# Kernel optimization log

Measured on AMD Instinct MI355X. Metric: run time of the kernel, lower is better.

Reference implementation:

```python
import jax, jax.numpy as jnp
import numpy as np

NEG_INF = float('-inf')


def setup_inputs() -> dict:
    key = jax.random.key(0)
    k1, k2, k3 = jax.random.split(key, 3)
    B, V = 256, 128000
    logits = jax.random.normal(k1, (B, V), dtype=jnp.float32) * 4.0
    # per-row top-k in [1, V]; k == V means top-k disabled for that row
    k = jax.random.randint(k2, (B,), 1, V + 1, dtype=jnp.int32)
    # per-row top-p in a realistic sampling range
    p = jax.random.uniform(k3, (B,), dtype=jnp.float32, minval=0.5, maxval=0.99)
    return {"logits": logits, "k": k, "p": p}


def reference(logits, k, p):
    """Faithful JAX port of vLLM apply_top_k_top_p (sort-based fallback).

    logits: [B, V] float32; k: [B] int (1..V, V => no top-k); p: [B] float (0,1].
    Returns masked logits [B, V] with filtered entries set to -inf.
    """
    B, V = logits.shape
    # ascending sort, as in torch: logits.sort(dim=-1, descending=False)
    idx = jnp.argsort(logits, axis=-1)                       # [B, V]
    logits_sort = jnp.take_along_axis(logits, idx, axis=-1)  # [B, V]

    # ---- top-k: threshold is the (V-k)-th smallest value; k==V -> idx 0 -> min,
    # so nothing is masked (strict '<' comparison), matching torch semantics.
    tk_idx = (V - k).astype(jnp.int32)[:, None]              # [B, 1]
    tk_thresh = jnp.take_along_axis(logits_sort, tk_idx, axis=-1)
    logits_sort = jnp.where(logits_sort < tk_thresh, NEG_INF, logits_sort)

    # ---- top-p: drop smallest-probability prefix with cumulative mass <= 1-p
    probs = jax.nn.softmax(logits_sort, axis=-1)
    top_p_mask = jnp.cumsum(probs, axis=-1) <= (1.0 - p)[:, None]
    top_p_mask = top_p_mask.at[:, -1].set(False)  # always keep the max logit
    logits_sort = jnp.where(top_p_mask, NEG_INF, logits_sort)

    # scatter masked sorted logits back to original positions (idx is a permutation)
    out = jnp.zeros_like(logits).at[jnp.arange(B)[:, None], idx].set(logits_sort)
    return out
```

## Files before the change

kernel.cpp:

```cpp
#include <hip/hip_runtime.h>

typedef unsigned long long u64;
typedef unsigned u32;
typedef float f32x4 __attribute__((ext_vector_type(4)));

#define VDIM   128000
#define NF4    32000
#define NROWS  256
#define NB     2048
#define NSEG   16
#define SEGW   768
#define CAPTOT (NSEG*SEGW)
#define CAPCHK 12288
#define CNTSH  47
#define EMASK  ((1ull<<CNTSH)-1ull)

#define MASKED_VAL -1.0e38f

__device__ __forceinline__ u32 f2key(float x){
  u32 u=__float_as_uint(x);
  return (u&0x80000000u)? ~u : (u|0x80000000u);
}
__device__ __forceinline__ float key2f(u32 k){
  u32 u=(k&0x80000000u)?(k&0x7FFFFFFFu):~k;
  return __uint_as_float(u);
}
__device__ __forceinline__ u64 expfx(float x){
  return (u64)(__expf(x)*8192.0f);
}

template<typename T>
__device__ __forceinline__ void block_scan_lds(T* a,int n){
  __shared__ T wsum[16];
  const int tid=threadIdx.x, lane=tid&63, wid=tid>>6;
  __syncthreads();
  const int chunk=n>>4;
  const int base=wid*chunk;
  T carry=(T)0;
  for(int c=0;c<chunk;c+=64){
    T v=a[base+c+lane];
    #pragma unroll
    for(int s=1;s<64;s<<=1){T t=__shfl_up(v,(unsigned)s);if(lane>=s)v+=t;}
    v+=carry;
    a[base+c+lane]=v;
    carry=__shfl(v,63);
  }
  if(lane==0)wsum[wid]=carry;
  __syncthreads();
  if(tid<64){
    T v=(tid<16)?wsum[tid]:(T)0;
    #pragma unroll
    for(int s=1;s<16;s<<=1){T t=__shfl_up(v,(unsigned)s);if(lane>=s)v+=t;}
    if(tid<16)wsum[tid]=v;
  }
  __syncthreads();
  if(wid>0){
    T off=wsum[wid-1];
    for(int c=0;c<chunk;c+=64)a[base+c+lane]+=off;
  }
  __syncthreads();
}

__device__ void gather(const float4* src,u32* ent,u32* wc,u32* fl,
                       int binA,int lo,int hi){
  const int tid=threadIdx.x, wid=tid>>6;
  if(tid<NSEG)wc[tid]=0u;
  if(tid==0){fl[0]=0u;fl[1]=0u;}
  __syncthreads();
  u32* seg=ent+wid*SEGW;
  for(int base=tid;base<NF4;base+=8192){
    float4 buf[8];
    #pragma unroll
    for(int u=0;u<8;u++){int i=base+u*1024;if(i<NF4)buf[u]=src[i];}
    #pragma unroll
    for(int u=0;u<8;u++){
      int i=base+u*1024;
      if(i<NF4){
        float xs[4]={buf[u].x,buf[u].y,buf[u].z,buf[u].w};
        #pragma unroll
        for(int c=0;c<4;c++){
          u32 key=f2key(xs[c]);
          int bin=(int)(key>>21);
          if(bin==binA||(bin>=lo&&bin<=hi)){
            u32 pos=atomicAdd(&wc[wid],1u);
            if(pos<SEGW)seg[pos]=key;
          }
        }
      }
    }
  }
  __syncthreads();
  if(tid<NSEG&&wc[tid]>(u32)SEGW)atomicOr(&fl[0],1u);
  __syncthreads();
  if(fl[0]){
    if(tid<NSEG)wc[tid]=0u;
    __syncthreads();
    for(int base=tid;base<NF4;base+=8192){
      float4 buf[8];
      #pragma unroll
      for(int u=0;u<8;u++){int i=base+u*1024;if(i<NF4)buf[u]=src[i];}
      #pragma unroll
      for(int u=0;u<8;u++){
        int i=base+u*1024;
        if(i<NF4){
          float xs[4]={buf[u].x,buf[u].y,buf[u].z,buf[u].w};
          #pragma unroll
          for(int c=0;c<4;c++){
            u32 key=f2key(xs[c]);
            int bin=(int)(key>>21);
            if(bin==binA||(bin>=lo&&bin<=hi)){
              u32 off=atomicAdd(&fl[1],1u);
              if(off<(u32)CAPTOT)ent[off]=key;
            }
          }
        }
      }
    }
    __syncthreads();
    if(tid<NSEG){
      int n=(int)min(fl[1],(u32)CAPTOT);
      int c0=n-tid*SEGW; c0=c0<0?0:(c0>SEGW?SEGW:c0);
      wc[tid]=(u32)c0;
    }
    __syncthreads();
  }else{
    __syncthreads();
  }
}

__device__ void refine_p(const float4* src,const u32* ent,const u32* wc,
                         u64* hR,int* si,u64* sw,
                         int bp,int bk,u32 K,u64 P0,double target,
                         u32* KPo,int* jso){
  const int tid=threadIdx.x;
  const bool fK=(bp==bk);
  if(tid==0){si[0]=-1;si[1]=-1;si[2]=0;si[5]=0;}
  for(int i=tid;i<NB;i+=1024)hR[i]=0ull;
  __syncthreads();
  for(int s=0;s<NSEG;s++){
    const int cN=(int)wc[s]; const u32* sp=ent+s*SEGW;
    for(int t=tid;t<cN;t+=1024){
      u32 key=sp[t];
      if((int)(key>>21)==bp&&(!fK||key>=K))
        atomicAdd(&hR[(key>>10)&0x7FFu],expfx(key2f(key)));
    }
  }
  block_scan_lds(hR,NB);
  for(int b=tid;b<NB;b+=1024){
    u64 cpre=P0+(b?hR[b-1]:0ull), cumb=P0+hR[b];
    if((double)cpre<=target&&target<(double)cumb){si[0]=b;sw[0]=cpre;}
  }
  __syncthreads();
  bool maskall=false;
  int b2=si[0];
  if(b2<0){
    maskall=true;
    for(int b=tid;b<NB;b+=1024){u64 pm=b?hR[b-1]:0ull;if(hR[b]>pm)atomicMax(&si[0],b);}
    __syncthreads();
    b2=si[0];
    if(tid==0&&b2>=0)sw[0]=P0+(b2>0?hR[b2-1]:0ull);
    __syncthreads();
    if(b2<0){*KPo=0u;*jso=-1;return;}
  }
  const u64 S2=sw[0];
  __syncthreads();
  hR[tid]=0ull;
  __syncthreads();
  for(int s=0;s<NSEG;s++){
    const int cN=(int)wc[s]; const u32* sp=ent+s*SEGW;
    for(int t=tid;t<cN;t+=1024){
      u32 key=sp[t];
      if((int)(key>>21)==bp&&(!fK||key>=K)&&(int)((key>>10)&0x7FFu)==b2)
        atomicAdd(&hR[key&0x3FFu],expfx(key2f(key)));
    }
  }
  block_scan_lds(hR,1024);
  if(!maskall&&tid<1024){
    u64 cpre=S2+(tid?hR[tid-1]:0ull), cumb=S2+hR[tid];
    if((double)cpre<=target&&target<(double)cumb)si[1]=tid;
  }
  __syncthreads();
  int low=si[1];
  if(low<0){
    maskall=true;
    if(tid<1024){u64 pm=tid?hR[tid-1]:0ull;if(hR[tid]>pm)atomicMax(&si[1],tid);}
    __syncthreads();
    low=si[1];
    if(low<0){*KPo=0u;*jso=-1;return;}
  }
  const u64 S3=S2+(low?hR[low-1]:0ull);
  const u32 KP=((u32)bp<<21)|((u32)b2<<10)|(u32)low;
  for(int s=0;s<NSEG;s++){
    const int cN=(int)wc[s]; const u32* sp=ent+s*SEGW;
    for(int t=tid;t<cN;t+=1024)if(sp[t]==KP)atomicAdd(&si[2],1);
  }
  __syncthreads();
  const int mm=min(si[2],4096);
  const u64 efx=expfx(key2f(KP));
  int r;
  if(maskall)r=mm;
  else if(efx==0ull)r=0;
  else{
    double f=(target-(double)S3)/(double)efx;
    r=(f<0.0)?0:(int)f;
    if(r>mm)r=mm;
  }
  int js=-1;
  if(r>0){
    __syncthreads();
    u32* tb=(u32*)hR;
    for(int i=tid;i<NF4;i+=1024){
      float4 v=src[i];
      float xs[4]={v.x,v.y,v.z,v.w};
      #pragma unroll
      for(int c=0;c<4;c++){
        if(f2key(xs[c])==KP){int pos=atomicAdd(&si[5],1);if(pos<2048)tb[pos]=(u32)(4*i+c);}
      }
    }
    __syncthreads();
    const int mc=min(si[5],2048);
    if(tid==0){
      if(r>=mc){
        u32 mx=0u;for(int q=0;q<mc;q++)mx=max(mx,tb[q]);
        si[3]=(int)mx;
      }else{
        int last=-1;
        for(int t2=0;t2<r;t2++){
          u32 mn=0xFFFFFFFFu;
          for(int q=0;q<mc;q++){u32 vi=tb[q];if((int)vi>last&&vi<mn)mn=vi;}
          last=(int)mn;
        }
        si[3]=last;
      }
    }
    __syncthreads();
    js=si[3];
  }
  if(tid==0)si[4]=(int)KP;
  __syncthreads();
  *KPo=(u32)si[4];*jso=js;
}

__global__ __launch_bounds__(1024) void k_fused(const float* __restrict__ lg,
    const int* __restrict__ karr,const float* __restrict__ parr,
    float* __restrict__ out){
  __shared__ u64 hA[NB];
  __shared__ u64 hR[NB];
  __shared__ u32 ent[CAPTOT];
  __shared__ u32 wc[NSEG];
  __shared__ u32 fl[2];
  __shared__ int si[12];
  __shared__ u64 sw[4];
  const int row=blockIdx.x, tid=threadIdx.x;
  const float4* src=(const float4*)(lg+(size_t)row*VDIM);

  for(int i=tid;i<NB;i+=1024)hA[i]=0ull;
  if(tid==0){si[0]=-1;si[1]=NB;si[2]=NB;si[3]=-1;si[4]=-1;si[5]=-1;}
  __syncthreads();
  for(int base=tid;base<NF4;base+=8192){
    float4 buf[8];
    #pragma unroll
    for(int u=0;u<8;u++){int i=base+u*1024;if(i<NF4)buf[u]=src[i];}
    #pragma unroll
    for(int u=0;u<8;u++){
      int i=base+u*1024;
      if(i<NF4){
        float xs[4]={buf[u].x,buf[u].y,buf[u].z,buf[u].w};
        #pragma unroll
        for(int c=0;c<4;c++){
          u32 key=f2key(xs[c]);
          atomicAdd(&hA[key>>21],(1ull<<CNTSH)+expfx(xs[c]));
        }
      }
    }
  }
  block_scan_lds(hA,NB);
  const int vk=VDIM-karr[row];
  for(int b=tid;b<NB;b+=1024){
    int pm1=b?(int)(hA[b-1]>>CNTSH):0, cm=(int)(hA[b]>>CNTSH);
    if(pm1<=vk&&vk<cm)si[0]=b;
  }
  __syncthreads();
  const int bk=si[0];
  const u64 Ebk=hA[bk]&EMASK;
  const u64 Ebkm1=bk?(hA[bk-1]&EMASK):0ull;
  const u64 Etot=hA[NB-1]&EMASK;
  const u64 tail=Etot-Ebk, Mbk=Ebk-Ebkm1;
  const int cntbk=(int)(hA[bk]>>CNTSH)-(bk?(int)(hA[bk-1]>>CNTSH):0);
  const int kprime=(int)(hA[bk]>>CNTSH)-vk;
  const float p=parr[row];
  const double th_max=(double)(1.0f-p)*(double)tail+(double)Ebk;
  const double th_min=th_max-(double)p*(double)Mbk;
  for(int b=tid;b<NB;b+=1024){
    double Eb=(double)(hA[b]&EMASK);
    if(Eb>th_min)atomicMin(&si[1],b);
    if(Eb>th_max)atomicMin(&si[2],b);
  }
  __syncthreads();
  int lo=si[1],hi=si[2];
  if(lo>=NB)lo=NB-1;
  if(hi>=NB)hi=NB-1;
  lo=max(bk,lo-1); hi=min(NB-1,hi+1); if(hi<lo)hi=lo;
  long long cr=(long long)(hA[hi]>>CNTSH)-(lo?(long long)(hA[lo-1]>>CNTSH):0ll);
  long long tot=cr+((lo==bk)?0ll:(long long)cntbk);
  const int comb=(tot<=(long long)CAPCHK)?1:0;
  gather(src,ent,wc,fl,bk,comb?lo:1,comb?hi:0);
  for(int i=tid;i<NB;i+=1024)hR[i]=0ull;
  __syncthreads();
  for(int s=0;s<NSEG;s++){
    const int cN=(int)wc[s]; const u32* sp=ent+s*SEGW;
    for(int t=tid;t<cN;t+=1024){
      u32 key=sp[t];
      if((int)(key>>21)==bk)
        atomicAdd(&hR[(key>>10)&0x7FFu],(1ull<<CNTSH)+expfx(key2f(key)));
    }
  }
  block_scan_lds(hR,NB);
  int t2=cntbk-kprime;if(t2<0)t2=0;
  for(int b=tid;b<NB;b+=1024){
    int pm1=b?(int)(hR[b-1]>>CNTSH):0, cm=(int)(hR[b]>>CNTSH);
    if(pm1<=t2&&t2<cm)si[3]=b;
  }
  __syncthreads();
  const int b2=(si[3]<0)?0:si[3];
  const int k2v=(int)(hR[b2]>>CNTSH)-t2;
  const u64 E2above=(hR[NB-1]&EMASK)-(hR[b2]&EMASK);
  __syncthreads();
  hR[tid]=0ull;
  __syncthreads();
  for(int s=0;s<NSEG;s++){
    const int cN=(int)wc[s]; const u32* sp=ent+s*SEGW;
    for(int t=tid;t<cN;t+=1024){
      u32 key=sp[t];
      if((int)(key>>21)==bk&&(int)((key>>10)&0x7FFu)==b2)
        atomicAdd(&hR[key&0x3FFu],(1ull<<CNTSH)+expfx(key2f(key)));
    }
  }
  block_scan_lds(hR,1024);
  const int nb2=(int)(hR[1023]>>CNTSH);
  int t3=nb2-k2v;if(t3<0)t3=0;
  if(tid<1024){
    int pm1=tid?(int)(hR[tid-1]>>CNTSH):0, cm=(int)(hR[tid]>>CNTSH);
    if(pm1<=t3&&t3<cm)si[4]=tid;
  }
  __syncthreads();
  const int lowk=(si[4]<0)?0:si[4];
  const u32 K=((u32)bk<<21)|((u32)b2<<10)|(u32)lowk;
  const u64 E3above=(hR[1023]&EMASK)-(lowk?(hR[lowk-1]&EMASK):0ull);
  const u64 kept=E2above+E3above;
  const double target=(double)(1.0f-p)*(double)(kept+tail);
  __syncthreads();
  for(int b=bk+tid;b<NB;b+=1024){
    u64 cpre=(b==bk)?0ull:(kept+((hA[b-1]&EMASK)-Ebk));
    u64 cumb=kept+((b>bk)?((hA[b]&EMASK)-Ebk):0ull);
    if((double)cpre<=target&&target<(double)cumb){si[5]=b;sw[0]=cpre;}
  }
  __syncthreads();
  const int bp=si[5];
  u32 KP=0u; int js=-1;
  if(bp>=0){
    const u64 P0=sw[0];
    const bool inset=(bp==bk)||(comb&&bp>=lo&&bp<=hi);
    if(!inset){
      __syncthreads();
      gather(src,ent,wc,fl,bp,1,0);
    }
    refine_p(src,ent,wc,hR,si+6,sw+1,bp,bk,K,P0,target,&KP,&js);
  }
  __syncthreads();
  f32x4* dst=(f32x4*)(out+(size_t)row*VDIM);
  for(int base=tid;base<NF4;base+=8192){
    float4 buf[8];
    #pragma unroll
    for(int u=0;u<8;u++){int i=base+u*1024;if(i<NF4)buf[u]=src[i];}
    #pragma unroll
    for(int u=0;u<8;u++){
      int i=base+u*1024;
      if(i<NF4){
        float xs[4]={buf[u].x,buf[u].y,buf[u].z,buf[u].w};
        f32x4 o;
        #pragma unroll
        for(int c=0;c<4;c++){
          u32 key=f2key(xs[c]);
          bool msk=(key<K)||(key<KP)||(key==KP&&(int)(4*i+c)<=js);
          o[c]=msk?MASKED_VAL:xs[c];
        }
        __builtin_nontemporal_store(o,dst+i);
      }
    }
  }
}

extern "C" void kernel_launch(void* const* d_in,const int* in_sizes,int n_in,
                              void* d_out,int out_size,void* d_ws,size_t ws_size,
                              hipStream_t stream){
  const float* lg=(const float*)d_in[0];
  const int*   karr=(const int*)d_in[1];
  const float* parr=(const float*)d_in[2];
  float* out=(float*)d_out;
  (void)d_ws;(void)ws_size;(void)in_sizes;(void)n_in;(void)out_size;
  k_fused<<<dim3(NROWS),dim3(1024),0,stream>>>(lg,karr,parr,out);
}
```

Measured before the change: 119.5 us.

## Fuse speculative output write into gather pass and fix up candidates only

In the combined case, the candidate-gather pass now also writes the output row. Elements in bins below the candidate range are written as masked, and all others are written unchanged. Candidate positions are kept in a new shared-memory array. When the final top-p threshold bin lies inside the gathered range, the closing full read-and-write pass is replaced by a scatter that rewrites only the candidate entries. This removes one full read of each row from global memory in the common case. It costs an extra 48KB of LDS and scattered, uncoalesced writes that overwrite values just stored by other threads.

```diff
diff --git a/kernel.cpp b/kernel.cpp
--- a/kernel.cpp
+++ b/kernel.cpp
@@ -61,13 +61,14 @@
   __syncthreads();
 }
 
-__device__ void gather(const float4* src,u32* ent,u32* wc,u32* fl,
-                       int binA,int lo,int hi){
+__device__ void gather(const float4* src,f32x4* dst,u32* ent,u32* pse,
+                       u32* wc,u32* fl,int binA,int lo,int hi,int stream){
   const int tid=threadIdx.x, wid=tid>>6;
   if(tid<NSEG)wc[tid]=0u;
   if(tid==0){fl[0]=0u;fl[1]=0u;}
   __syncthreads();
   u32* seg=ent+wid*SEGW;
+  u32* sgp=pse+wid*SEGW;
   for(int base=tid;base<NF4;base+=8192){
     float4 buf[8];
     #pragma unroll
@@ -77,15 +78,19 @@
       int i=base+u*1024;
       if(i<NF4){
         float xs[4]={buf[u].x,buf[u].y,buf[u].z,buf[u].w};
+        f32x4 o;
         #pragma unroll
         for(int c=0;c<4;c++){
           u32 key=f2key(xs[c]);
           int bin=(int)(key>>21);
-          if(bin==binA||(bin>=lo&&bin<=hi)){
+          bool cand=(bin==binA)||(bin>=lo&&bin<=hi);
+          if(cand){
             u32 pos=atomicAdd(&wc[wid],1u);
-            if(pos<SEGW)seg[pos]=key;
+            if(pos<(u32)SEGW){seg[pos]=key;sgp[pos]=(u32)(4*i+c);}
           }
+          o[c]=(!cand&&bin<lo)?MASKED_VAL:xs[c];
         }
+        if(stream)__builtin_nontemporal_store(o,dst+i);
       }
     }
   }
@@ -110,7 +115,7 @@
             int bin=(int)(key>>21);
             if(bin==binA||(bin>=lo&&bin<=hi)){
               u32 off=atomicAdd(&fl[1],1u);
-              if(off<(u32)CAPTOT)ent[off]=key;
+              if(off<(u32)CAPTOT){ent[off]=key;pse[off]=(u32)(4*i+c);}
             }
           }
         }
@@ -247,12 +252,14 @@
   __shared__ u64 hA[NB];
   __shared__ u64 hR[NB];
   __shared__ u32 ent[CAPTOT];
+  __shared__ u32 pse[CAPTOT];
   __shared__ u32 wc[NSEG];
   __shared__ u32 fl[2];
   __shared__ int si[12];
   __shared__ u64 sw[4];
   const int row=blockIdx.x, tid=threadIdx.x;
   const float4* src=(const float4*)(lg+(size_t)row*VDIM);
+  f32x4* dst=(f32x4*)(out+(size_t)row*VDIM);
 
   for(int i=tid;i<NB;i+=1024)hA[i]=0ull;
   if(tid==0){si[0]=-1;si[1]=NB;si[2]=NB;si[3]=-1;si[4]=-1;si[5]=-1;}
@@ -304,7 +311,7 @@
   long long cr=(long long)(hA[hi]>>CNTSH)-(lo?(long long)(hA[lo-1]>>CNTSH):0ll);
   long long tot=cr+((lo==bk)?0ll:(long long)cntbk);
   const int comb=(tot<=(long long)CAPCHK)?1:0;
-  gather(src,ent,wc,fl,bk,comb?lo:1,comb?hi:0);
+  gather(src,dst,ent,pse,wc,fl,bk,comb?lo:1,comb?hi:0,comb);
   for(int i=tid;i<NB;i+=1024)hR[i]=0ull;
   __syncthreads();
   for(int s=0;s<NSEG;s++){
@@ -363,29 +370,42 @@
     const bool inset=(bp==bk)||(comb&&bp>=lo&&bp<=hi);
     if(!inset){
       __syncthreads();
-      gather(src,ent,wc,fl,bp,1,0);
+      gather(src,dst,ent,pse,wc,fl,bp,1,0,0);
     }
     refine_p(src,ent,wc,hR,si+6,sw+1,bp,bk,K,P0,target,&KP,&js);
   }
   __syncthreads();
-  f32x4* dst=(f32x4*)(out+(size_t)row*VDIM);
-  for(int base=tid;base<NF4;base+=8192){
-    float4 buf[8];
-    #pragma unroll
-    for(int u=0;u<8;u++){int i=base+u*1024;if(i<NF4)buf[u]=src[i];}
-    #pragma unroll
-    for(int u=0;u<8;u++){
-      int i=base+u*1024;
-      if(i<NF4){
-        float xs[4]={buf[u].x,buf[u].y,buf[u].z,buf[u].w};
-        f32x4 o;
-        #pragma unroll
-        for(int c=0;c<4;c++){
-          u32 key=f2key(xs[c]);
-          bool msk=(key<K)||(key<KP)||(key==KP&&(int)(4*i+c)<=js);
-          o[c]=msk?MASKED_VAL:xs[c];
+  const bool dofix=comb&&bp>=lo&&bp<=hi&&KP!=0u;
+  if(dofix){
+    float* op=out+(size_t)row*VDIM;
+    for(int s=0;s<NSEG;s++){
+      const int cN=(int)wc[s];
+      const u32* sp=ent+s*SEGW; const u32* pp=pse+s*SEGW;
+      for(int t=tid;t<cN;t+=1024){
+        u32 key=sp[t]; u32 ps=pp[t];
+        bool msk=(key<K)||(key<KP)||(key==KP&&(int)ps<=js);
+        op[ps]=msk?MASKED_VAL:key2f(key);
+      }
+    }
+  }else{
+    for(int base=tid;base<NF4;base+=8192){
+      float4 buf[8];
+      #pragma unroll
+      for(int u=0;u<8;u++){int i=base+u*1024;if(i<NF4)buf[u]=src[i];}
+      #pragma unroll
+      for(int u=0;u<8;u++){
+        int i=base+u*1024;
+        if(i<NF4){
+          float xs[4]={buf[u].x,buf[u].y,buf[u].z,buf[u].w};
+          f32x4 o;
+          #pragma unroll
+          for(int c=0;c<4;c++){
+            u32 key=f2key(xs[c]);
+            bool msk=(key<K)||(key<KP)||(key==KP&&(int)(4*i+c)<=js);
+            o[c]=msk?MASKED_VAL:xs[c];
+          }
+          __builtin_nontemporal_store(o,dst+i);
         }
-        __builtin_nontemporal_store(o,dst+i);
       }
     }
   }
```

Measured after the change: 130.2 us. +8.9%, slower.

## Split fused kernel into histogram, threshold, and write kernels with half-row blocks

Applied to the files above, without the earlier changes.

Splits the single per-row kernel into three launches. A histogram kernel uses two blocks per row, each over half the row, with partial histograms written to workspace. The main kernel sums them and finds thresholds, and a write kernel applies the mask with two blocks per row. The aim is to spread the bandwidth-heavy passes over 512 blocks with lighter shared-memory use, so more blocks fit per CU than the 256-block fused kernel allows, at the cost of extra launches and workspace round trips.

```diff
diff --git a/kernel.cpp b/kernel.cpp
--- a/kernel.cpp
+++ b/kernel.cpp
@@ -6,6 +6,7 @@
 
 #define VDIM   128000
 #define NF4    32000
+#define NF4H   16000
 #define NROWS  256
 #define NB     2048
 #define NSEG   16
@@ -241,9 +242,39 @@
   *KPo=(u32)si[4];*jso=js;
 }
 
-__global__ __launch_bounds__(1024) void k_fused(const float* __restrict__ lg,
+__global__ __launch_bounds__(1024,8) void k_hist(const float* __restrict__ lg,
+    u64* __restrict__ ws){
+  __shared__ u64 h[NB];
+  const int row=(int)blockIdx.x>>1, half=(int)blockIdx.x&1, tid=threadIdx.x;
+  const float4* src=(const float4*)(lg+(size_t)row*VDIM);
+  for(int i=tid;i<NB;i+=1024)h[i]=0ull;
+  __syncthreads();
+  const int h0=half*NF4H, h1=h0+NF4H;
+  for(int base=h0+tid;base<h1;base+=8192){
+    float4 buf[8];
+    #pragma unroll
+    for(int u=0;u<8;u++){int i=base+u*1024;if(i<h1)buf[u]=src[i];}
+    #pragma unroll
+    for(int u=0;u<8;u++){
+      int i=base+u*1024;
+      if(i<h1){
+        float xs[4]={buf[u].x,buf[u].y,buf[u].z,buf[u].w};
+        #pragma unroll
+        for(int c=0;c<4;c++){
+          u32 key=f2key(xs[c]);
+          atomicAdd(&h[key>>21],(1ull<<CNTSH)+expfx(xs[c]));
+        }
+      }
+    }
+  }
+  __syncthreads();
+  u64* dst=ws+(size_t)blockIdx.x*NB;
+  for(int i=tid;i<NB;i+=1024)dst[i]=h[i];
+}
+
+__global__ __launch_bounds__(1024) void k_main(const float* __restrict__ lg,
     const int* __restrict__ karr,const float* __restrict__ parr,
-    float* __restrict__ out){
+    u64* __restrict__ ws){
   __shared__ u64 hA[NB];
   __shared__ u64 hR[NB];
   __shared__ u32 ent[CAPTOT];
@@ -254,26 +285,12 @@
   const int row=blockIdx.x, tid=threadIdx.x;
   const float4* src=(const float4*)(lg+(size_t)row*VDIM);
 
-  for(int i=tid;i<NB;i+=1024)hA[i]=0ull;
+  {
+    const u64* p0=ws+(size_t)(row*2+0)*NB;
+    const u64* p1=ws+(size_t)(row*2+1)*NB;
+    for(int b=tid;b<NB;b+=1024)hA[b]=p0[b]+p1[b];
+  }
   if(tid==0){si[0]=-1;si[1]=NB;si[2]=NB;si[3]=-1;si[4]=-1;si[5]=-1;}
-  __syncthreads();
-  for(int base=tid;base<NF4;base+=8192){
-    float4 buf[8];
-    #pragma unroll
-    for(int u=0;u<8;u++){int i=base+u*1024;if(i<NF4)buf[u]=src[i];}
-    #pragma unroll
-    for(int u=0;u<8;u++){
-      int i=base+u*1024;
-      if(i<NF4){
-        float xs[4]={buf[u].x,buf[u].y,buf[u].z,buf[u].w};
-        #pragma unroll
-        for(int c=0;c<4;c++){
-          u32 key=f2key(xs[c]);
-          atomicAdd(&hA[key>>21],(1ull<<CNTSH)+expfx(xs[c]));
-        }
-      }
-    }
-  }
   block_scan_lds(hA,NB);
   const int vk=VDIM-karr[row];
   for(int b=tid;b<NB;b+=1024){
@@ -368,15 +385,28 @@
     refine_p(src,ent,wc,hR,si+6,sw+1,bp,bk,K,P0,target,&KP,&js);
   }
   __syncthreads();
+  if(tid==0){
+    u32* res=(u32*)(ws+(size_t)(2*NROWS)*NB)+row*4;
+    res[0]=K; res[1]=KP; res[2]=(u32)js;
+  }
+}
+
+__global__ __launch_bounds__(1024,8) void k_write(const float* __restrict__ lg,
+    const u64* __restrict__ ws,float* __restrict__ out){
+  const int row=(int)blockIdx.x>>1, half=(int)blockIdx.x&1, tid=threadIdx.x;
+  const float4* src=(const float4*)(lg+(size_t)row*VDIM);
   f32x4* dst=(f32x4*)(out+(size_t)row*VDIM);
-  for(int base=tid;base<NF4;base+=8192){
+  const u32* res=(const u32*)(ws+(size_t)(2*NROWS)*NB)+row*4;
+  const u32 K=res[0], KP=res[1]; const int js=(int)res[2];
+  const int h0=half*NF4H, h1=h0+NF4H;
+  for(int base=h0+tid;base<h1;base+=8192){
     float4 buf[8];
     #pragma unroll
-    for(int u=0;u<8;u++){int i=base+u*1024;if(i<NF4)buf[u]=src[i];}
+    for(int u=0;u<8;u++){int i=base+u*1024;if(i<h1)buf[u]=src[i];}
     #pragma unroll
     for(int u=0;u<8;u++){
       int i=base+u*1024;
-      if(i<NF4){
+      if(i<h1){
         float xs[4]={buf[u].x,buf[u].y,buf[u].z,buf[u].w};
         f32x4 o;
         #pragma unroll
@@ -398,6 +428,9 @@
   const int*   karr=(const int*)d_in[1];
   const float* parr=(const float*)d_in[2];
   float* out=(float*)d_out;
-  (void)d_ws;(void)ws_size;(void)in_sizes;(void)n_in;(void)out_size;
-  k_fused<<<dim3(NROWS),dim3(1024),0,stream>>>(lg,karr,parr,out);
-}
+  u64* ws=(u64*)d_ws;
+  (void)ws_size;(void)in_sizes;(void)n_in;(void)out_size;
+  k_hist <<<dim3(2*NROWS),dim3(1024),0,stream>>>(lg,ws);
+  k_main <<<dim3(NROWS)  ,dim3(1024),0,stream>>>(lg,karr,parr,ws);
+  k_write<<<dim3(2*NROWS),dim3(1024),0,stream>>>(lg,ws,out);
+}
```

After: 168.0 us. 40.6% more time.

## Double-buffer row streaming loads and flatten segment scans

Applied to the files above, without the earlier changes.

Replaces the load-then-process loops over the row with a double-buffered schedule: the next 8-float4 burst is loaded while the current one is histogrammed, gathered or written out, with tail indices clamped so the loads are unconditional. The per-segment nested loops over the LDS candidate buffer become one flat loop over the full capacity with a per-entry bounds check, which removes serial segment iteration at the cost of visiting empty slots. The launch bounds now also request 4 waves per SIMD, which raises register pressure from the doubled buffers.

```diff
diff --git a/kernel.cpp b/kernel.cpp
--- a/kernel.cpp
+++ b/kernel.cpp
@@ -29,6 +29,12 @@
   return (u64)(__expf(x)*8192.0f);
 }
 
+__device__ __forceinline__ void ldburst(const float4* __restrict__ src,
+                                        int t0,float4* b){
+  #pragma unroll
+  for(int u=0;u<8;u++){int i=t0+u*1024;i=(i<NF4)?i:(NF4-1);b[u]=src[i];}
+}
+
 template<typename T>
 __device__ __forceinline__ void block_scan_lds(T* a,int n){
   __shared__ T wsum[16];
@@ -61,6 +67,26 @@
   __syncthreads();
 }
 
+__device__ __forceinline__ void gatherburst(const float4* b,int t0,
+    int binA,int lo,int hi,u32* wc,u32* seg,int wid){
+  #pragma unroll
+  for(int u=0;u<8;u++){
+    int i=t0+u*1024;
+    if(i<NF4){
+      float xs[4]={b[u].x,b[u].y,b[u].z,b[u].w};
+      #pragma unroll
+      for(int c=0;c<4;c++){
+        u32 key=f2key(xs[c]);
+        int bin=(int)(key>>21);
+        if(bin==binA||(bin>=lo&&bin<=hi)){
+          u32 pos=atomicAdd(&wc[wid],1u);
+          if(pos<SEGW)seg[pos]=key;
+        }
+      }
+    }
+  }
+}
+
 __device__ void gather(const float4* src,u32* ent,u32* wc,u32* fl,
                        int binA,int lo,int hi){
   const int tid=threadIdx.x, wid=tid>>6;
@@ -68,26 +94,16 @@
   if(tid==0){fl[0]=0u;fl[1]=0u;}
   __syncthreads();
   u32* seg=ent+wid*SEGW;
-  for(int base=tid;base<NF4;base+=8192){
-    float4 buf[8];
-    #pragma unroll
-    for(int u=0;u<8;u++){int i=base+u*1024;if(i<NF4)buf[u]=src[i];}
-    #pragma unroll
-    for(int u=0;u<8;u++){
-      int i=base+u*1024;
-      if(i<NF4){
-        float xs[4]={buf[u].x,buf[u].y,buf[u].z,buf[u].w};
-        #pragma unroll
-        for(int c=0;c<4;c++){
-          u32 key=f2key(xs[c]);
-          int bin=(int)(key>>21);
-          if(bin==binA||(bin>=lo&&bin<=hi)){
-            u32 pos=atomicAdd(&wc[wid],1u);
-            if(pos<SEGW)seg[pos]=key;
-          }
-        }
-      }
-    }
+  {
+    float4 bA[8],bB[8];
+    ldburst(src,tid,bA);
+    ldburst(src,tid+8192,bB);
+    gatherburst(bA,tid,binA,lo,hi,wc,seg,wid);
+    ldburst(src,tid+16384,bA);
+    gatherburst(bB,tid+8192,binA,lo,hi,wc,seg,wid);
+    ldburst(src,tid+24576,bB);
+    gatherburst(bA,tid+16384,binA,lo,hi,wc,seg,wid);
+    gatherburst(bB,tid+24576,binA,lo,hi,wc,seg,wid);
   }
   __syncthreads();
   if(tid<NSEG&&wc[tid]>(u32)SEGW)atomicOr(&fl[0],1u);
@@ -137,10 +153,10 @@
   if(tid==0){si[0]=-1;si[1]=-1;si[2]=0;si[5]=0;}
   for(int i=tid;i<NB;i+=1024)hR[i]=0ull;
   __syncthreads();
-  for(int s=0;s<NSEG;s++){
-    const int cN=(int)wc[s]; const u32* sp=ent+s*SEGW;
-    for(int t=tid;t<cN;t+=1024){
-      u32 key=sp[t];
+  for(int t=tid;t<CAPTOT;t+=1024){
+    int s=t/SEGW;
+    if((u32)(t-s*SEGW)<wc[s]){
+      u32 key=ent[t];
       if((int)(key>>21)==bp&&(!fK||key>=K))
         atomicAdd(&hR[(key>>10)&0x7FFu],expfx(key2f(key)));
     }
@@ -166,10 +182,10 @@
   __syncthreads();
   hR[tid]=0ull;
   __syncthreads();
-  for(int s=0;s<NSEG;s++){
-    const int cN=(int)wc[s]; const u32* sp=ent+s*SEGW;
-    for(int t=tid;t<cN;t+=1024){
-      u32 key=sp[t];
+  for(int t=tid;t<CAPTOT;t+=1024){
+    int s=t/SEGW;
+    if((u32)(t-s*SEGW)<wc[s]){
+      u32 key=ent[t];
       if((int)(key>>21)==bp&&(!fK||key>=K)&&(int)((key>>10)&0x7FFu)==b2)
         atomicAdd(&hR[key&0x3FFu],expfx(key2f(key)));
     }
@@ -190,9 +206,9 @@
   }
   const u64 S3=S2+(low?hR[low-1]:0ull);
   const u32 KP=((u32)bp<<21)|((u32)b2<<10)|(u32)low;
-  for(int s=0;s<NSEG;s++){
-    const int cN=(int)wc[s]; const u32* sp=ent+s*SEGW;
-    for(int t=tid;t<cN;t+=1024)if(sp[t]==KP)atomicAdd(&si[2],1);
+  for(int t=tid;t<CAPTOT;t+=1024){
+    int s=t/SEGW;
+    if((u32)(t-s*SEGW)<wc[s]&&ent[t]==KP)atomicAdd(&si[2],1);
   }
   __syncthreads();
   const int mm=min(si[2],4096);
@@ -241,7 +257,40 @@
   *KPo=(u32)si[4];*jso=js;
 }
 
-__global__ __launch_bounds__(1024) void k_fused(const float* __restrict__ lg,
+__device__ __forceinline__ void histburst(const float4* b,int t0,u64* hA){
+  #pragma unroll
+  for(int u=0;u<8;u++){
+    int i=t0+u*1024;
+    if(i<NF4){
+      float xs[4]={b[u].x,b[u].y,b[u].z,b[u].w};
+      #pragma unroll
+      for(int c=0;c<4;c++){
+        u32 key=f2key(xs[c]);
+        atomicAdd(&hA[key>>21],(1ull<<CNTSH)+expfx(xs[c]));
+      }
+    }
+  }
+}
+__device__ __forceinline__ void writeburst(const float4* b,int t0,
+    u32 K,u32 KP,int js,f32x4* dst){
+  #pragma unroll
+  for(int u=0;u<8;u++){
+    int i=t0+u*1024;
+    if(i<NF4){
+      float xs[4]={b[u].x,b[u].y,b[u].z,b[u].w};
+      f32x4 o;
+      #pragma unroll
+      for(int c=0;c<4;c++){
+        u32 key=f2key(xs[c]);
+        bool msk=(key<K)||(key<KP)||(key==KP&&(int)(4*i+c)<=js);
+        o[c]=msk?MASKED_VAL:xs[c];
+      }
+      __builtin_nontemporal_store(o,dst+i);
+    }
+  }
+}
+
+__global__ __launch_bounds__(1024,4) void k_fused(const float* __restrict__ lg,
     const int* __restrict__ karr,const float* __restrict__ parr,
     float* __restrict__ out){
   __shared__ u64 hA[NB];
@@ -257,22 +306,16 @@
   for(int i=tid;i<NB;i+=1024)hA[i]=0ull;
   if(tid==0){si[0]=-1;si[1]=NB;si[2]=NB;si[3]=-1;si[4]=-1;si[5]=-1;}
   __syncthreads();
-  for(int base=tid;base<NF4;base+=8192){
-    float4 buf[8];
-    #pragma unroll
-    for(int u=0;u<8;u++){int i=base+u*1024;if(i<NF4)buf[u]=src[i];}
-    #pragma unroll
-    for(int u=0;u<8;u++){
-      int i=base+u*1024;
-      if(i<NF4){
-        float xs[4]={buf[u].x,buf[u].y,buf[u].z,buf[u].w};
-        #pragma unroll
-        for(int c=0;c<4;c++){
-          u32 key=f2key(xs[c]);
-          atomicAdd(&hA[key>>21],(1ull<<CNTSH)+expfx(xs[c]));
-        }
-      }
-    }
+  {
+    float4 bA[8],bB[8];
+    ldburst(src,tid,bA);
+    ldburst(src,tid+8192,bB);
+    histburst(bA,tid,hA);
+    ldburst(src,tid+16384,bA);
+    histburst(bB,tid+8192,hA);
+    ldburst(src,tid+24576,bB);
+    histburst(bA,tid+16384,hA);
+    histburst(bB,tid+24576,hA);
   }
   block_scan_lds(hA,NB);
   const int vk=VDIM-karr[row];
@@ -307,10 +350,10 @@
   gather(src,ent,wc,fl,bk,comb?lo:1,comb?hi:0);
   for(int i=tid;i<NB;i+=1024)hR[i]=0ull;
   __syncthreads();
-  for(int s=0;s<NSEG;s++){
-    const int cN=(int)wc[s]; const u32* sp=ent+s*SEGW;
-    for(int t=tid;t<cN;t+=1024){
-      u32 key=sp[t];
+  for(int t=tid;t<CAPTOT;t+=1024){
+    int s=t/SEGW;
+    if((u32)(t-s*SEGW)<wc[s]){
+      u32 key=ent[t];
       if((int)(key>>21)==bk)
         atomicAdd(&hR[(key>>10)&0x7FFu],(1ull<<CNTSH)+expfx(key2f(key)));
     }
@@ -328,10 +371,10 @@
   __syncthreads();
   hR[tid]=0ull;
   __syncthreads();
-  for(int s=0;s<NSEG;s++){
-    const int cN=(int)wc[s]; const u32* sp=ent+s*SEGW;
-    for(int t=tid;t<cN;t+=1024){
-      u32 key=sp[t];
+  for(int t=tid;t<CAPTOT;t+=1024){
+    int s=t/SEGW;
+    if((u32)(t-s*SEGW)<wc[s]){
+      u32 key=ent[t];
       if((int)(key>>21)==bk&&(int)((key>>10)&0x7FFu)==b2)
         atomicAdd(&hR[key&0x3FFu],(1ull<<CNTSH)+expfx(key2f(key)));
     }
@@ -369,25 +412,16 @@
   }
   __syncthreads();
   f32x4* dst=(f32x4*)(out+(size_t)row*VDIM);
-  for(int base=tid;base<NF4;base+=8192){
-    float4 buf[8];
-    #pragma unroll
-    for(int u=0;u<8;u++){int i=base+u*1024;if(i<NF4)buf[u]=src[i];}
-    #pragma unroll
-    for(int u=0;u<8;u++){
-      int i=base+u*1024;
-      if(i<NF4){
-        float xs[4]={buf[u].x,buf[u].y,buf[u].z,buf[u].w};
-        f32x4 o;
-        #pragma unroll
-        for(int c=0;c<4;c++){
-          u32 key=f2key(xs[c]);
-          bool msk=(key<K)||(key<KP)||(key==KP&&(int)(4*i+c)<=js);
-          o[c]=msk?MASKED_VAL:xs[c];
-        }
-        __builtin_nontemporal_store(o,dst+i);
-      }
-    }
+  {
+    float4 bA[8],bB[8];
+    ldburst(src,tid,bA);
+    ldburst(src,tid+8192,bB);
+    writeburst(bA,tid,K,KP,js,dst);
+    ldburst(src,tid+16384,bA);
+    writeburst(bB,tid+8192,K,KP,js,dst);
+    ldburst(src,tid+24576,bB);
+    writeburst(bA,tid+16384,K,KP,js,dst);
+    writeburst(bB,tid+24576,K,KP,js,dst);
   }
 }
 
```

Result: slower. 131.1 us (+9.7%).
